# Optimization experiments

Hardware: AMD Instinct MI355X
Metric: run time of the kernel (lower is better)

The kernel has to match this reference:

```python
import jax, jax.numpy as jnp
import numpy as np
from jax import lax

T, B, H_IN, H_HID = 2048, 64, 256, 256


def _orth(key, shape):
    a = jax.random.normal(key, shape, jnp.float32)
    if shape[0] >= shape[1]:
        q, _ = jnp.linalg.qr(a)
    else:
        q, _ = jnp.linalg.qr(a.T)
        q = q.T
    return q[: shape[0], : shape[1]].astype(jnp.float32)


def setup_inputs() -> dict:
    key = jax.random.key(0)
    ks = jax.random.split(key, 6)
    x = jax.random.normal(ks[0], (T, B, H_IN), jnp.float32)
    rnn_hxs = jax.random.normal(ks[1], (1, B, H_HID), jnp.float32)
    batch_mask = jax.random.randint(ks[2], (T, B), 0, 2).astype(bool)
    # force column 0 fully valid so pad_packed max length == T (static shape)
    batch_mask = batch_mask.at[:, 0].set(True)
    w_ih = _orth(ks[3], (3 * H_HID, H_IN))   # [3H, H_in] gates r,z,n
    w_hh = _orth(ks[4], (3 * H_HID, H_HID))
    b_ih = jnp.zeros((3 * H_HID,), jnp.float32)  # constant_(0) init
    b_hh = jnp.zeros((3 * H_HID,), jnp.float32)
    return {"x": x, "rnn_hxs": rnn_hxs, "batch_mask": batch_mask,
            "w_ih": w_ih, "w_hh": w_hh, "b_ih": b_ih, "b_hh": b_hh}


def _gru_ragged(x, h0, batch_mask, w_ih, w_hh, b_ih, b_hh):
    Tn, Bn, _ = x.shape
    Hh = h0.shape[-1]
    mask = batch_mask
    lens = mask.sum(0)                      # [B] per-column valid lengths
    # --- gather/pack: move valid steps of each column to the front ---
    rank = jnp.cumsum(mask, axis=0) - mask  # compact position per (t,b)
    rank_m = jnp.where(mask, rank, Tn)      # invalid rows -> dump row Tn
    cols = jnp.broadcast_to(jnp.arange(Bn), (Tn, Bn))
    compact = jnp.zeros((Tn + 1, Bn, x.shape[-1]), x.dtype)
    compact = compact.at[rank_m, cols].set(x)[:Tn]
    # --- GRU over compact sequences; h frozen past each column's length ---
    gi = jnp.einsum('tbi,gi->tbg', compact, w_ih) + b_ih  # [T,B,3H]
    valid = jnp.arange(Tn)[:, None] < lens[None, :]       # [T,B]

    def step(h, inp):
        gi_t, v = inp
        gh = jnp.einsum('bh,gh->bg', h, w_hh) + b_hh
        r = jax.nn.sigmoid(gi_t[:, :Hh] + gh[:, :Hh])
        z = jax.nn.sigmoid(gi_t[:, Hh:2 * Hh] + gh[:, Hh:2 * Hh])
        n = jnp.tanh(gi_t[:, 2 * Hh:] + r * gh[:, 2 * Hh:])
        h_new = (1.0 - z) * n + z * h
        h_out = jnp.where(v[:, None], h_new, h)
        out = jnp.where(v[:, None], h_new, 0.0)  # pad_packed zero padding
        return h_out, out

    hT, scores = lax.scan(step, h0, (gi, valid))  # scores [T,B,Hh]
    # --- masked_scatter: true positions of dest (row-major t,b order)
    # consume consecutive H-rows of the flattened padded scores ---
    mflat = mask.reshape(-1)
    flat_rank = jnp.cumsum(mflat) - mflat            # exclusive cumsum
    src = scores.reshape(Tn * Bn, Hh)
    gathered = src[flat_rank]                        # [T*B, Hh]
    out = jnp.where(mflat[:, None], gathered, 0.0).reshape(Tn, Bn, Hh)
    return out, hT


def reference(x, rnn_hxs, batch_mask, w_ih, w_hh, b_ih, b_hh):
    scores, hT = _gru_ragged(x, rnn_hxs[0], batch_mask, w_ih, w_hh, b_ih, b_hh)
    return scores, hT[None]
```

## Files before the change

### kernel.cpp

```cpp
#include <hip/hip_runtime.h>
#include <cstdint>
#include <cstddef>

#define T_LEN 2048
#define B_N   64
#define H_INP 256
#define H_HID 256
#define G3    768
#define M_ROWS (T_LEN * B_N)
#define SCH   8

typedef _Float16 f16;
typedef _Float16 f16x2 __attribute__((ext_vector_type(2)));
typedef _Float16 f16x8 __attribute__((ext_vector_type(8)));
typedef float    f32x4 __attribute__((ext_vector_type(4)));

static __device__ __forceinline__ float fdot2f(uint32_t a, uint32_t b, float c) {
#if __has_builtin(__builtin_amdgcn_fdot2)
  return __builtin_amdgcn_fdot2(__builtin_bit_cast(f16x2, a),
                                __builtin_bit_cast(f16x2, b), c, false);
#else
  f16x2 av = __builtin_bit_cast(f16x2, a);
  f16x2 bv = __builtin_bit_cast(f16x2, b);
  return c + (float)av.x * (float)bv.x + (float)av.y * (float)bv.y;
#endif
}

__global__ void k_zero(float4* __restrict__ p, int n4) {
  int i = blockIdx.x * blockDim.x + threadIdx.x;
  int stride = gridDim.x * blockDim.x;
  float4 z; z.x = z.y = z.z = z.w = 0.f;
  for (; i < n4; i += stride) p[i] = z;
}

__global__ void k_cvt(const float2* __restrict__ s, f16x2* __restrict__ d, int n2) {
  int i = blockIdx.x * blockDim.x + threadIdx.x;
  int stride = gridDim.x * blockDim.x;
  for (; i < n2; i += stride) {
    float2 v = s[i];
    f16x2 p; p.x = (f16)v.x; p.y = (f16)v.y;
    d[i] = p;
  }
}

__global__ __launch_bounds__(64) void k_prep_col(const int* __restrict__ mask,
                                                 unsigned short* __restrict__ tidx,
                                                 int* __restrict__ lens) {
  const int b = blockIdx.x;
  const int lane = threadIdx.x;
  unsigned short* tp = tidx + b * T_LEN;
  int base = 0;
  for (int c = 0; c < T_LEN / 64; ++c) {
    int t = c * 64 + lane;
    bool m = mask[t * B_N + b] != 0;
    unsigned long long bal = __ballot(m);
    int pc = __popcll(bal & ((1ull << lane) - 1ull));
    if (m) tp[base + pc] = (unsigned short)t;
    base += __popcll(bal);
  }
  if (lane == 0) lens[b] = base;
}

__global__ __launch_bounds__(256) void k_rowcnt(const int* __restrict__ mask,
                                                int* __restrict__ rowcnt) {
  int g = blockIdx.x * 256 + threadIdx.x;
  int t = g >> 6, lane = g & 63;
  bool m = mask[t * B_N + lane] != 0;
  unsigned long long bal = __ballot(m);
  if (lane == 0) rowcnt[t] = __popcll(bal);
}

__global__ __launch_bounds__(512) void k_rowpref(const int* __restrict__ rowcnt,
                                                 int* __restrict__ rowpref,
                                                 int* __restrict__ ntru) {
  const int tid = threadIdx.x;
  const int lane = tid & 63, w = tid >> 6;
  int4 v = ((const int4*)rowcnt)[tid];
  int s = v.x + v.y + v.z + v.w;
  int incl = s;
  for (int d = 1; d < 64; d <<= 1) {
    int t = __shfl_up(incl, d, 64);
    if (lane >= d) incl += t;
  }
  __shared__ int wt[8], wo[8];
  if (lane == 63) wt[w] = incl;
  __syncthreads();
  if (tid == 0) {
    int run = 0;
    for (int i = 0; i < 8; ++i) { wo[i] = run; run += wt[i]; }
    ntru[0] = run;
  }
  __syncthreads();
  int base = wo[w] + incl - s;
  int4 o; o.x = base; o.y = base + v.x; o.z = o.y + v.y; o.w = o.z + v.z;
  ((int4*)rowpref)[tid] = o;
}

__global__ __launch_bounds__(256) void k_inv(const int* __restrict__ mask,
                                             const int* __restrict__ rowpref,
                                             int* __restrict__ inv) {
  int g = blockIdx.x * 256 + threadIdx.x;
  int t = g >> 6, lane = g & 63;
  bool m = mask[t * B_N + lane] != 0;
  unsigned long long bal = __ballot(m);
  int r = rowpref[t] + __popcll(bal & ((1ull << lane) - 1ull));
  if (m) inv[r] = t * B_N + lane;
}

__global__ __launch_bounds__(256) void k_invT(const int* __restrict__ inv,
                                              const int* __restrict__ ntru,
                                              int* __restrict__ invT) {
  int j = blockIdx.x * 256 + threadIdx.x;
  int v = (j < ntru[0]) ? inv[j] : -1;
  invT[(j & 63) * T_LEN + (j >> 6)] = v;
}

__global__ __launch_bounds__(256) void k_gemm(const f16* __restrict__ X,
                                              const f16* __restrict__ W,
                                              const float* __restrict__ bias,
                                              f16* __restrict__ GI) {
  const int lane = threadIdx.x & 63;
  const int wave = threadIdx.x >> 6;
  const int m0 = blockIdx.x * 64 + wave * 16;
  const int n0 = blockIdx.y * 64;
  const int idx16 = lane & 15;
  const int kofs  = (lane >> 4) * 8;

  const f16* ap  = X + (size_t)(m0 + idx16) * H_INP + kofs;
  const f16* bp0 = W + (size_t)(n0 + idx16) * H_INP + kofs;

  f32x4 acc[4] = { {0,0,0,0}, {0,0,0,0}, {0,0,0,0}, {0,0,0,0} };
#pragma unroll
  for (int kt = 0; kt < 8; ++kt) {
    f16x8 a = *(const f16x8*)(ap + kt * 32);
#pragma unroll
    for (int nt = 0; nt < 4; ++nt) {
      f16x8 bb = *(const f16x8*)(bp0 + (size_t)nt * 16 * H_INP + kt * 32);
      acc[nt] = __builtin_amdgcn_mfma_f32_16x16x32_f16(a, bb, acc[nt], 0, 0, 0);
    }
  }
  const int mbase = m0 + (lane >> 4) * 4;
#pragma unroll
  for (int nt = 0; nt < 4; ++nt) {
    const int col = n0 + nt * 16 + idx16;
    const float bv = bias[col];
#pragma unroll
    for (int r = 0; r < 4; ++r)
      GI[(size_t)(mbase + r) * G3 + col] = (f16)(acc[nt][r] + bv);
  }
}

__global__ __launch_bounds__(768, 3) void k_scan(const f16* __restrict__ Whh,
                                                 const f16* __restrict__ GI,
                                                 const float* __restrict__ h0,
                                                 const float* __restrict__ bhh,
                                                 const unsigned short* __restrict__ tidx,
                                                 const int* __restrict__ lens,
                                                 const int* __restrict__ invT,
                                                 float* __restrict__ out) {
  const int b = blockIdx.x;
  const int tid = threadIdx.x;
  const int o = tid & 7;
  const int rbase = (tid >> 3) << 3;

  __shared__ f16      GIbuf[2][SCH * G3];
  __shared__ float    outb[SCH * H_HID];
  __shared__ float    ghs[2 * H_HID];
  __shared__ uint32_t hpad[160];
  __shared__ unsigned short tcol[T_LEN];
  __shared__ int      invcol[T_LEN];

  const int L = lens[b];

  uint4 wq[8][4];
#pragma unroll
  for (int i = 0; i < 8; ++i) {
    const uint4* wp = (const uint4*)(Whh + (size_t)(rbase + i) * H_HID + 32 * o);
#pragma unroll
    for (int q = 0; q < 4; ++q) wq[i][q] = wp[q];
  }
  const float bias = bhh[tid];

  for (int i = tid; i < T_LEN; i += 768) {
    tcol[i] = tidx[b * T_LEN + i];
    invcol[i] = invT[b * T_LEN + i];
  }
  float h_reg = 0.f;
  if (tid < H_HID) {
    h_reg = h0[b * H_HID + tid];
    ((f16*)hpad)[40 * (tid >> 5) + (tid & 31)] = (f16)h_reg;
  }

  const int r_s = tid / 96;
  const int o_s = (tid % 96) * 16;
  const char* GIc = (const char*)GI;
  uint4 pref = {0, 0, 0, 0};

  __syncthreads();

  if (r_s < L) {
    int t = tcol[r_s];
    pref = *(const uint4*)(GIc + ((size_t)t * B_N + b) * (G3 * 2) + o_s);
  }

  const int nchunks = (L + SCH - 1) >> 3;
  for (int n = 0; n < nchunks; ++n) {
    const int par = n & 1;
    if (n * SCH + r_s < L)
      *(uint4*)((char*)GIbuf[par] + tid * 16) = pref;
    {
      int kk = (n + 1) * SCH + r_s;
      if (kk < L) {
        int t = tcol[kk];
        pref = *(const uint4*)(GIc + ((size_t)t * B_N + b) * (G3 * 2) + o_s);
      }
    }
    if (n > 0 && tid < 512) {
      int r = tid >> 6, c4 = (tid & 63) << 2;
      int kk = (n - 1) * SCH + r;
      if (kk < L) {
        int iv = invcol[kk];
        if (iv >= 0)
          *(float4*)(out + (size_t)iv * H_HID + c4) = *(const float4*)(outb + r * H_HID + c4);
      }
    }

    const int smax = (L - n * SCH < SCH) ? (L - n * SCH) : SCH;
    for (int s = 0; s < smax; ++s) {
      float a0 = 0.f, a1 = 0.f, a2 = 0.f, a3 = 0.f;
      float a4 = 0.f, a5 = 0.f, a6 = 0.f, a7 = 0.f;
#pragma unroll
      for (int q = 0; q < 4; ++q) {
        uint4 hv = *(const uint4*)(hpad + 20 * o + 4 * q);
        a0 = fdot2f(wq[0][q].x, hv.x, a0); a0 = fdot2f(wq[0][q].y, hv.y, a0);
        a0 = fdot2f(wq[0][q].z, hv.z, a0); a0 = fdot2f(wq[0][q].w, hv.w, a0);
        a1 = fdot2f(wq[1][q].x, hv.x, a1); a1 = fdot2f(wq[1][q].y, hv.y, a1);
        a1 = fdot2f(wq[1][q].z, hv.z, a1); a1 = fdot2f(wq[1][q].w, hv.w, a1);
        a2 = fdot2f(wq[2][q].x, hv.x, a2); a2 = fdot2f(wq[2][q].y, hv.y, a2);
        a2 = fdot2f(wq[2][q].z, hv.z, a2); a2 = fdot2f(wq[2][q].w, hv.w, a2);
        a3 = fdot2f(wq[3][q].x, hv.x, a3); a3 = fdot2f(wq[3][q].y, hv.y, a3);
        a3 = fdot2f(wq[3][q].z, hv.z, a3); a3 = fdot2f(wq[3][q].w, hv.w, a3);
        a4 = fdot2f(wq[4][q].x, hv.x, a4); a4 = fdot2f(wq[4][q].y, hv.y, a4);
        a4 = fdot2f(wq[4][q].z, hv.z, a4); a4 = fdot2f(wq[4][q].w, hv.w, a4);
        a5 = fdot2f(wq[5][q].x, hv.x, a5); a5 = fdot2f(wq[5][q].y, hv.y, a5);
        a5 = fdot2f(wq[5][q].z, hv.z, a5); a5 = fdot2f(wq[5][q].w, hv.w, a5);
        a6 = fdot2f(wq[6][q].x, hv.x, a6); a6 = fdot2f(wq[6][q].y, hv.y, a6);
        a6 = fdot2f(wq[6][q].z, hv.z, a6); a6 = fdot2f(wq[6][q].w, hv.w, a6);
        a7 = fdot2f(wq[7][q].x, hv.x, a7); a7 = fdot2f(wq[7][q].y, hv.y, a7);
        a7 = fdot2f(wq[7][q].z, hv.z, a7); a7 = fdot2f(wq[7][q].w, hv.w, a7);
      }
      const bool h4 = (tid & 4), h2 = (tid & 2), h1 = (tid & 1);
      float se, ns, b0, b1, b2, b3, c0, c1;
      se = h4 ? a4 : a0; ns = h4 ? a0 : a4; b0 = se + __shfl_xor(ns, 4);
      se = h4 ? a5 : a1; ns = h4 ? a1 : a5; b1 = se + __shfl_xor(ns, 4);
      se = h4 ? a6 : a2; ns = h4 ? a2 : a6; b2 = se + __shfl_xor(ns, 4);
      se = h4 ? a7 : a3; ns = h4 ? a3 : a7; b3 = se + __shfl_xor(ns, 4);
      se = h2 ? b2 : b0; ns = h2 ? b0 : b2; c0 = se + __shfl_xor(ns, 2);
      se = h2 ? b3 : b1; ns = h2 ? b1 : b3; c1 = se + __shfl_xor(ns, 2);
      se = h1 ? c1 : c0; ns = h1 ? c0 : c1;
      const float gh = se + __shfl_xor(ns, 1) + bias;
      if (tid >= H_HID) ghs[tid - H_HID] = gh;
      __syncthreads();
      if (tid < H_HID) {
        const f16* gib = GIbuf[par] + s * G3;
        const float gi0 = (float)gib[tid];
        const float gi1 = (float)gib[H_HID + tid];
        const float gi2 = (float)gib[2 * H_HID + tid];
        const float ghz = ghs[tid];
        const float ghn = ghs[H_HID + tid];
        const float rg = __builtin_amdgcn_rcpf(1.f + __expf(-(gi0 + gh)));
        const float zg = __builtin_amdgcn_rcpf(1.f + __expf(-(gi1 + ghz)));
        const float xx = gi2 + rg * ghn;
        const float ng = 1.f - 2.f * __builtin_amdgcn_rcpf(1.f + __expf(2.f * xx));
        const float hn = (1.f - zg) * ng + zg * h_reg;
        h_reg = hn;
        ((f16*)hpad)[40 * (tid >> 5) + (tid & 31)] = (f16)hn;
        outb[s * H_HID + tid] = hn;
      }
      __syncthreads();
    }
  }
  if (L > 0 && tid < 512) {
    const int nc = nchunks - 1;
    int r = tid >> 6, c4 = (tid & 63) << 2;
    int kk = nc * SCH + r;
    if (kk < L) {
      int iv = invcol[kk];
      if (iv >= 0)
        *(float4*)(out + (size_t)iv * H_HID + c4) = *(const float4*)(outb + r * H_HID + c4);
    }
  }
  if (tid < H_HID)
    out[(size_t)M_ROWS * H_HID + (size_t)b * H_HID + tid] = h_reg;
}

extern "C" void kernel_launch(void* const* d_in, const int* in_sizes, int n_in,
                              void* d_out, int out_size, void* d_ws, size_t ws_size,
                              hipStream_t stream) {
  const float* x    = (const float*)d_in[0];
  const float* h0   = (const float*)d_in[1];
  const int*   mask = (const int*)d_in[2];
  const float* wih  = (const float*)d_in[3];
  const float* whh  = (const float*)d_in[4];
  const float* bih  = (const float*)d_in[5];
  const float* bhh  = (const float*)d_in[6];
  float* out = (float*)d_out;

  char* ws = (char*)d_ws;
  f16* X16   = (f16*)(ws + 0);
  int* invT  = (int*)(ws + 0);
  f16* Wih16 = (f16*)(ws + 67108864);
  f16* Whh16 = (f16*)(ws + 67502080);
  f16* GI    = (f16*)(ws + 67895296);
  unsigned short* tidx = (unsigned short*)(ws + 269221888);
  int* rowcnt  = (int*)(ws + 269484032);
  int* rowpref = (int*)(ws + 269492224);
  int* inv   = (int*)(ws + 269746176);
  int* lens  = (int*)(ws + 270270464);
  int* ntru  = (int*)(ws + 270270720);

  hipLaunchKernelGGL(k_zero, dim3(4096), dim3(256), 0, stream,
                     (float4*)d_out, out_size / 4);
  hipLaunchKernelGGL(k_cvt, dim3(4096), dim3(256), 0, stream,
                     (const float2*)x, (f16x2*)X16, M_ROWS * H_INP / 2);
  hipLaunchKernelGGL(k_cvt, dim3(96), dim3(256), 0, stream,
                     (const float2*)wih, (f16x2*)Wih16, G3 * H_INP / 2);
  hipLaunchKernelGGL(k_cvt, dim3(96), dim3(256), 0, stream,
                     (const float2*)whh, (f16x2*)Whh16, G3 * H_INP / 2);
  hipLaunchKernelGGL(k_prep_col, dim3(B_N), dim3(64), 0, stream,
                     mask, tidx, lens);
  hipLaunchKernelGGL(k_rowcnt, dim3(512), dim3(256), 0, stream, mask, rowcnt);
  hipLaunchKernelGGL(k_rowpref, dim3(1), dim3(512), 0, stream,
                     rowcnt, rowpref, ntru);
  hipLaunchKernelGGL(k_inv, dim3(512), dim3(256), 0, stream,
                     mask, rowpref, inv);
  hipLaunchKernelGGL(k_gemm, dim3(M_ROWS / 64, G3 / 64), dim3(256), 0, stream,
                     X16, Wih16, bih, GI);
  hipLaunchKernelGGL(k_invT, dim3(512), dim3(256), 0, stream,
                     inv, ntru, invT);
  hipLaunchKernelGGL(k_scan, dim3(B_N), dim3(768), 0, stream,
                     Whh16, GI, h0, bhh, tidx, lens, invT, out);
}
```

Before: 3.413 ms.

## Restructure GRU scan to 512 threads with DPP reductions and async LDS loads

```diff
diff --git a/kernel.cpp b/kernel.cpp
--- a/kernel.cpp
+++ b/kernel.cpp
@@ -23,6 +23,42 @@
   f16x2 av = __builtin_bit_cast(f16x2, a);
   f16x2 bv = __builtin_bit_cast(f16x2, b);
   return c + (float)av.x * (float)bv.x + (float)av.y * (float)bv.y;
+#endif
+}
+
+template <int CTRL>
+static __device__ __forceinline__ float dppf(float v) {
+  return __builtin_bit_cast(float,
+      __builtin_amdgcn_update_dpp(0, __builtin_bit_cast(int, v), CTRL, 0xf, 0xf, true));
+}
+static __device__ __forceinline__ float x4sel(float v, bool hi4) {
+  float lo = dppf<0x104>(v);
+  float hi = dppf<0x114>(v);
+  return hi4 ? hi : lo;
+}
+static __device__ __forceinline__ float mrg4(float lo, float hi, bool h) {
+  float mine = h ? hi : lo;
+  float th   = h ? lo : hi;
+  return mine + x4sel(th, h);
+}
+static __device__ __forceinline__ float mrg2(float lo, float hi, bool h) {
+  float mine = h ? hi : lo;
+  float th   = h ? lo : hi;
+  return mine + dppf<0x4E>(th);
+}
+static __device__ __forceinline__ float mrg1(float lo, float hi, bool h) {
+  float mine = h ? hi : lo;
+  float th   = h ? lo : hi;
+  return mine + dppf<0xB1>(th);
+}
+
+static __device__ __forceinline__ void gldl16(const void* g, void* ldsbase, void* ldsexact) {
+#if __has_builtin(__builtin_amdgcn_global_load_lds)
+  __builtin_amdgcn_global_load_lds((const __attribute__((address_space(1))) void*)g,
+                                   (__attribute__((address_space(3))) void*)ldsbase, 16, 0, 0);
+  (void)ldsexact;
+#else
+  *(uint4*)ldsexact = *(const uint4*)g;
 #endif
 }
 
@@ -126,6 +162,8 @@
   const int idx16 = lane & 15;
   const int kofs  = (lane >> 4) * 8;
 
+  __shared__ __align__(16) f16 st[4][16][72];
+
   const f16* ap  = X + (size_t)(m0 + idx16) * H_INP + kofs;
   const f16* bp0 = W + (size_t)(n0 + idx16) * H_INP + kofs;
 
@@ -139,49 +177,62 @@
       acc[nt] = __builtin_amdgcn_mfma_f32_16x16x32_f16(a, bb, acc[nt], 0, 0, 0);
     }
   }
-  const int mbase = m0 + (lane >> 4) * 4;
 #pragma unroll
   for (int nt = 0; nt < 4; ++nt) {
-    const int col = n0 + nt * 16 + idx16;
-    const float bv = bias[col];
+    const int col = nt * 16 + idx16;
+    const float bv = bias[n0 + col];
 #pragma unroll
     for (int r = 0; r < 4; ++r)
-      GI[(size_t)(mbase + r) * G3 + col] = (f16)(acc[nt][r] + bv);
-  }
-}
-
-__global__ __launch_bounds__(768, 3) void k_scan(const f16* __restrict__ Whh,
-                                                 const f16* __restrict__ GI,
-                                                 const float* __restrict__ h0,
-                                                 const float* __restrict__ bhh,
-                                                 const unsigned short* __restrict__ tidx,
-                                                 const int* __restrict__ lens,
-                                                 const int* __restrict__ invT,
-                                                 float* __restrict__ out) {
+      st[wave][(lane >> 4) * 4 + r][col] = (f16)(acc[nt][r] + bv);
+  }
+  {
+    const int row = lane >> 2, seg = lane & 3;
+    const uint4* sp = (const uint4*)&st[wave][row][seg * 16];
+    uint4 v0 = sp[0], v1 = sp[1];
+    uint4* gp = (uint4*)(GI + (size_t)(m0 + row) * G3 + n0 + seg * 16);
+    gp[0] = v0; gp[1] = v1;
+  }
+}
+
+__global__ __launch_bounds__(512)
+__attribute__((amdgpu_waves_per_eu(2, 2)))
+void k_scan(const f16* __restrict__ Whh,
+            const f16* __restrict__ GI,
+            const float* __restrict__ h0,
+            const float* __restrict__ bhh,
+            const unsigned short* __restrict__ tidx,
+            const int* __restrict__ lens,
+            const int* __restrict__ invT,
+            float* __restrict__ out) {
   const int b = blockIdx.x;
   const int tid = threadIdx.x;
   const int o = tid & 7;
-  const int rbase = (tid >> 3) << 3;
-
-  __shared__ f16      GIbuf[2][SCH * G3];
+  const int grp = tid >> 3;
+  const int rbase = grp * 12;
+  const bool o4 = (tid & 4) != 0, o2 = (tid & 2) != 0, o1 = (tid & 1) != 0;
+
+  __shared__ __align__(16) f16 GIbuf[2][SCH * G3];
   __shared__ float    outb[SCH * H_HID];
-  __shared__ float    ghs[2 * H_HID];
+  __shared__ float    ghs[G3];
   __shared__ uint32_t hpad[160];
   __shared__ unsigned short tcol[T_LEN];
   __shared__ int      invcol[T_LEN];
 
   const int L = lens[b];
 
-  uint4 wq[8][4];
-#pragma unroll
-  for (int i = 0; i < 8; ++i) {
+  uint4 wq[12][4];
+#pragma unroll
+  for (int i = 0; i < 12; ++i) {
     const uint4* wp = (const uint4*)(Whh + (size_t)(rbase + i) * H_HID + 32 * o);
 #pragma unroll
     for (int q = 0; q < 4; ++q) wq[i][q] = wp[q];
   }
-  const float bias = bhh[tid];
-
-  for (int i = tid; i < T_LEN; i += 768) {
+  const int rowA = rbase + o;
+  const int rowB = rbase + 8 + ((tid & 4) >> 1) + ((tid & 2) >> 1);
+  const float bA = bhh[rowA];
+  const float bB = bhh[rowB];
+
+  for (int i = tid; i < T_LEN; i += 512) {
     tcol[i] = tidx[b * T_LEN + i];
     invcol[i] = invT[b * T_LEN + i];
   }
@@ -190,32 +241,39 @@
     h_reg = h0[b * H_HID + tid];
     ((f16*)hpad)[40 * (tid >> 5) + (tid & 31)] = (f16)h_reg;
   }
-
-  const int r_s = tid / 96;
-  const int o_s = (tid % 96) * 16;
+  __syncthreads();
+
   const char* GIc = (const char*)GI;
-  uint4 pref = {0, 0, 0, 0};
-
-  __syncthreads();
-
-  if (r_s < L) {
-    int t = tcol[r_s];
-    pref = *(const uint4*)(GIc + ((size_t)t * B_N + b) * (G3 * 2) + o_s);
-  }
+  const int wavbase = (tid >> 6) << 10;
+
+  auto issue_chunk = [&](int m) {
+    {
+      int p = tid << 4;
+      int r = p / 1536;
+      int kk = m * SCH + r;
+      int t = tcol[kk < L ? kk : 0] & (T_LEN - 1);
+      const char* src = GIc + ((size_t)((t << 6) + b)) * 1536 + (p - r * 1536);
+      char* dbase = (char*)GIbuf[m & 1] + wavbase;
+      gldl16(src, dbase, (char*)GIbuf[m & 1] + p);
+    }
+    if (tid < 256) {
+      int p = 8192 + (tid << 4);
+      int r = p / 1536;
+      int kk = m * SCH + r;
+      int t = tcol[kk < L ? kk : 0] & (T_LEN - 1);
+      const char* src = GIc + ((size_t)((t << 6) + b)) * 1536 + (p - r * 1536);
+      char* dbase = (char*)GIbuf[m & 1] + 8192 + wavbase;
+      gldl16(src, dbase, (char*)GIbuf[m & 1] + p);
+    }
+  };
+
+  issue_chunk(0);
 
   const int nchunks = (L + SCH - 1) >> 3;
   for (int n = 0; n < nchunks; ++n) {
     const int par = n & 1;
-    if (n * SCH + r_s < L)
-      *(uint4*)((char*)GIbuf[par] + tid * 16) = pref;
-    {
-      int kk = (n + 1) * SCH + r_s;
-      if (kk < L) {
-        int t = tcol[kk];
-        pref = *(const uint4*)(GIc + ((size_t)t * B_N + b) * (G3 * 2) + o_s);
-      }
-    }
-    if (n > 0 && tid < 512) {
+    if (n + 1 < nchunks) issue_chunk(n + 1);
+    if (n > 0) {
       int r = tid >> 6, c4 = (tid & 63) << 2;
       int kk = (n - 1) * SCH + r;
       if (kk < L) {
@@ -225,50 +283,46 @@
       }
     }
 
-    const int smax = (L - n * SCH < SCH) ? (L - n * SCH) : SCH;
+    const int kbase = n * SCH;
+    const int smax = (L - kbase < SCH) ? (L - kbase) : SCH;
     for (int s = 0; s < smax; ++s) {
-      float a0 = 0.f, a1 = 0.f, a2 = 0.f, a3 = 0.f;
-      float a4 = 0.f, a5 = 0.f, a6 = 0.f, a7 = 0.f;
+      float aa[12];
+#pragma unroll
+      for (int i = 0; i < 12; ++i) aa[i] = 0.f;
 #pragma unroll
       for (int q = 0; q < 4; ++q) {
-        uint4 hv = *(const uint4*)(hpad + 20 * o + 4 * q);
-        a0 = fdot2f(wq[0][q].x, hv.x, a0); a0 = fdot2f(wq[0][q].y, hv.y, a0);
-        a0 = fdot2f(wq[0][q].z, hv.z, a0); a0 = fdot2f(wq[0][q].w, hv.w, a0);
-        a1 = fdot2f(wq[1][q].x, hv.x, a1); a1 = fdot2f(wq[1][q].y, hv.y, a1);
-        a1 = fdot2f(wq[1][q].z, hv.z, a1); a1 = fdot2f(wq[1][q].w, hv.w, a1);
-        a2 = fdot2f(wq[2][q].x, hv.x, a2); a2 = fdot2f(wq[2][q].y, hv.y, a2);
-        a2 = fdot2f(wq[2][q].z, hv.z, a2); a2 = fdot2f(wq[2][q].w, hv.w, a2);
-        a3 = fdot2f(wq[3][q].x, hv.x, a3); a3 = fdot2f(wq[3][q].y, hv.y, a3);
-        a3 = fdot2f(wq[3][q].z, hv.z, a3); a3 = fdot2f(wq[3][q].w, hv.w, a3);
-        a4 = fdot2f(wq[4][q].x, hv.x, a4); a4 = fdot2f(wq[4][q].y, hv.y, a4);
-        a4 = fdot2f(wq[4][q].z, hv.z, a4); a4 = fdot2f(wq[4][q].w, hv.w, a4);
-        a5 = fdot2f(wq[5][q].x, hv.x, a5); a5 = fdot2f(wq[5][q].y, hv.y, a5);
-        a5 = fdot2f(wq[5][q].z, hv.z, a5); a5 = fdot2f(wq[5][q].w, hv.w, a5);
-        a6 = fdot2f(wq[6][q].x, hv.x, a6); a6 = fdot2f(wq[6][q].y, hv.y, a6);
-        a6 = fdot2f(wq[6][q].z, hv.z, a6); a6 = fdot2f(wq[6][q].w, hv.w, a6);
-        a7 = fdot2f(wq[7][q].x, hv.x, a7); a7 = fdot2f(wq[7][q].y, hv.y, a7);
-        a7 = fdot2f(wq[7][q].z, hv.z, a7); a7 = fdot2f(wq[7][q].w, hv.w, a7);
+        uint4 hv = *((const uint4*)(hpad + 20 * o) + q);
+#pragma unroll
+        for (int i = 0; i < 12; ++i) {
+          aa[i] = fdot2f(wq[i][q].x, hv.x, aa[i]);
+          aa[i] = fdot2f(wq[i][q].y, hv.y, aa[i]);
+          aa[i] = fdot2f(wq[i][q].z, hv.z, aa[i]);
+          aa[i] = fdot2f(wq[i][q].w, hv.w, aa[i]);
+        }
       }
-      const bool h4 = (tid & 4), h2 = (tid & 2), h1 = (tid & 1);
-      float se, ns, b0, b1, b2, b3, c0, c1;
-      se = h4 ? a4 : a0; ns = h4 ? a0 : a4; b0 = se + __shfl_xor(ns, 4);
-      se = h4 ? a5 : a1; ns = h4 ? a1 : a5; b1 = se + __shfl_xor(ns, 4);
-      se = h4 ? a6 : a2; ns = h4 ? a2 : a6; b2 = se + __shfl_xor(ns, 4);
-      se = h4 ? a7 : a3; ns = h4 ? a3 : a7; b3 = se + __shfl_xor(ns, 4);
-      se = h2 ? b2 : b0; ns = h2 ? b0 : b2; c0 = se + __shfl_xor(ns, 2);
-      se = h2 ? b3 : b1; ns = h2 ? b1 : b3; c1 = se + __shfl_xor(ns, 2);
-      se = h1 ? c1 : c0; ns = h1 ? c0 : c1;
-      const float gh = se + __shfl_xor(ns, 1) + bias;
-      if (tid >= H_HID) ghs[tid - H_HID] = gh;
+      float b0 = mrg4(aa[0], aa[4], o4);
+      float b1 = mrg4(aa[1], aa[5], o4);
+      float b2 = mrg4(aa[2], aa[6], o4);
+      float b3 = mrg4(aa[3], aa[7], o4);
+      float c0 = mrg2(b0, b2, o2);
+      float c1 = mrg2(b1, b3, o2);
+      float ghA = mrg1(c0, c1, o1) + bA;
+      float d0 = mrg4(aa[8], aa[10], o4);
+      float d1 = mrg4(aa[9], aa[11], o4);
+      float e  = mrg2(d0, d1, o2);
+      float ghB = e + dppf<0xB1>(e) + bB;
+      ghs[rowA] = ghA;
+      ghs[rowB] = ghB;
       __syncthreads();
       if (tid < H_HID) {
         const f16* gib = GIbuf[par] + s * G3;
         const float gi0 = (float)gib[tid];
         const float gi1 = (float)gib[H_HID + tid];
         const float gi2 = (float)gib[2 * H_HID + tid];
-        const float ghz = ghs[tid];
-        const float ghn = ghs[H_HID + tid];
-        const float rg = __builtin_amdgcn_rcpf(1.f + __expf(-(gi0 + gh)));
+        const float ghr = ghs[tid];
+        const float ghz = ghs[H_HID + tid];
+        const float ghn = ghs[2 * H_HID + tid];
+        const float rg = __builtin_amdgcn_rcpf(1.f + __expf(-(gi0 + ghr)));
         const float zg = __builtin_amdgcn_rcpf(1.f + __expf(-(gi1 + ghz)));
         const float xx = gi2 + rg * ghn;
         const float ng = 1.f - 2.f * __builtin_amdgcn_rcpf(1.f + __expf(2.f * xx));
@@ -280,7 +334,7 @@
       __syncthreads();
     }
   }
-  if (L > 0 && tid < 512) {
+  if (L > 0) {
     const int nc = nchunks - 1;
     int r = tid >> 6, c4 = (tid & 63) << 2;
     int kk = nc * SCH + r;
@@ -338,6 +392,6 @@
                      X16, Wih16, bih, GI);
   hipLaunchKernelGGL(k_invT, dim3(512), dim3(256), 0, stream,
                      inv, ntru, invT);
-  hipLaunchKernelGGL(k_scan, dim3(B_N), dim3(768), 0, stream,
+  hipLaunchKernelGGL(k_scan, dim3(B_N), dim3(512), 0, stream,
                      Whh16, GI, h0, bhh, tidx, lens, invT, out);
 }
```

Measured after the change: 3.147 ms. 7.8% less time.
